# Optimization experiments

Measured on AMD Instinct MI355X. Metric: run time of the kernel, lower is better.

Reference implementation:

```python
import jax, jax.numpy as jnp
import numpy as np

PI = np.pi
ALPHA_MIN = 0.001
EXPR = 10  # mixture expressivity

B, D = 8192, 1024
T = D // 2  # transformed sites (odd indices); conditioner sites are even indices


def setup_inputs() -> dict:
    key = jax.random.key(0)
    k0, k1, k2 = jax.random.split(key, 3)
    z = jax.random.uniform(k0, (B, D), dtype=jnp.float32, minval=0.05, maxval=2 * PI - 0.05)
    H = 1024
    W1 = jax.random.normal(k1, (2 * T, H), dtype=jnp.float32) * (1.0 / np.sqrt(2 * T))
    b1 = jnp.zeros((H,), dtype=jnp.float32)
    W2 = jax.random.normal(k2, (H, T * EXPR * 3), dtype=jnp.float32) * (1.0 / np.sqrt(H))
    b2 = jnp.zeros((T * EXPR * 3,), dtype=jnp.float32)
    return {"z": z, "W1": W1, "b1": b1, "W2": W2, "b2": b2}


def _conditioner(cond, W1, b1, W2, b2):
    # angle embedding -> MLP -> (alpha, beta, rho) per transformed site / mixture comp
    feat = jnp.concatenate([jnp.cos(cond), jnp.sin(cond)], axis=-1)  # [B, 2T]
    h = jax.nn.relu(feat @ W1 + b1)
    out = (h @ W2 + b2).reshape(cond.shape[0], T, EXPR, 3)
    alpha = jax.nn.softplus(out[..., 0]) + ALPHA_MIN          # [B,T,E] >= alpha_min
    beta = out[..., 1]                                        # [B,T,E]
    rho = jax.nn.softmax(out[..., 2], axis=-1)                # [B,T,E] simplex
    return alpha, beta, rho


def _ncp(phi, alpha, beta, rho):
    # NCP diffeomorphism on (0, 2pi): mixture of 2*atan(alpha*tan((phi-pi)/2)+beta)+pi
    x = jnp.tan(0.5 * (phi - PI))[..., None]                  # [B,T,1]
    u = alpha * x + beta                                      # [B,T,E]
    h = 2.0 * jnp.arctan(u) + PI
    out = jnp.sum(rho * h, axis=-1)                           # [B,T]
    deriv = alpha * (1.0 + x * x) / (1.0 + u * u)             # dh/dphi per comp
    logabsdet = jnp.log(jnp.sum(rho * deriv, axis=-1))        # [B,T]
    return out, logabsdet


def reference(z, W1, b1, W2, b2):
    cond = z[:, 0::2]   # conditioner_mask (even sites)
    phi = z[:, 1::2]    # transformed_mask (odd sites)
    alpha, beta, rho = _conditioner(cond, W1, b1, W2, b2)
    out, ld = _ncp(phi, alpha, beta, rho)
    z_new = z.at[:, 1::2].set(out)
    log_det = jnp.sum(ld, axis=-1)  # [B]
    return z_new, log_det
```

## Files before the change

kernel.cpp:

```cpp
#include <hip/hip_runtime.h>
#include <hip/hip_bf16.h>
#include <cstdint>

#define PI_F 3.14159265358979323846f

typedef __attribute__((ext_vector_type(8))) short bf16x8;
typedef __attribute__((ext_vector_type(4))) float f32x4;

__device__ __forceinline__ void gload_lds16(const void* g, void* l) {
  __builtin_amdgcn_global_load_lds(
      (const __attribute__((address_space(1))) void*)g,
      (__attribute__((address_space(3))) void*)l, 16, 0, 0);
}

__global__ __launch_bounds__(256) void prep_feat_kernel(
    const float* __restrict__ z, __hip_bfloat16* __restrict__ feat,
    float* __restrict__ zout, float* __restrict__ logdet)
{
  int idx = blockIdx.x * 256 + threadIdx.x;
  int b = idx >> 9, j = idx & 511;
  float2 zz = ((const float2*)z)[idx];
  feat[(size_t)b * 1024 + j]       = __float2bfloat16(cosf(zz.x));
  feat[(size_t)b * 1024 + 512 + j] = __float2bfloat16(sinf(zz.x));
  zout[(size_t)b * 1024 + 2 * j]   = zz.x;
  if (idx < 8192) logdet[idx] = 0.f;
}

__global__ __launch_bounds__(256) void transpose_bf16_kernel(
    const float* __restrict__ src, __hip_bfloat16* __restrict__ dst, int R, int C)
{
  __shared__ float tile[32][33];
  int c0 = blockIdx.x * 32, r0 = blockIdx.y * 32;
  int x = threadIdx.x, y = threadIdx.y;
  #pragma unroll
  for (int i = 0; i < 32; i += 8)
    tile[y + i][x] = src[(size_t)(r0 + y + i) * C + c0 + x];
  __syncthreads();
  #pragma unroll
  for (int i = 0; i < 32; i += 8)
    dst[(size_t)(c0 + y + i) * R + r0 + x] = __float2bfloat16(tile[x][y + i]);
}

__global__ __launch_bounds__(256, 2) void gemm1_kernel(
    const __hip_bfloat16* __restrict__ A, const __hip_bfloat16* __restrict__ Bt,
    const float* __restrict__ bias, __hip_bfloat16* __restrict__ H)
{
  __shared__ __align__(16) char smem[32768];
  const int tid = threadIdx.x;
  const int lane = tid & 63;
  const int w = tid >> 6;
  const int m0 = blockIdx.x * 128;
  const int n0 = blockIdx.y * 128;
  const int lrow = lane >> 3;
  const int scol = ((lane & 7) ^ lrow) << 4;
  const int fofs0 = ((lane >> 4) << 4) ^ ((lane & 7) << 4);
  const int arow = w * 32 + (lane & 15);
  const int brow = (lane & 15);

  f32x4 acc[2][8];
  #pragma unroll
  for (int i = 0; i < 2; ++i)
    #pragma unroll
    for (int j = 0; j < 8; ++j) acc[i][j] = (f32x4){0.f, 0.f, 0.f, 0.f};

  const char* Abase = (const char*)A + (size_t)(m0 + lrow) * 2048 + scol;
  const char* Bbase = (const char*)Bt + (size_t)(n0 + lrow) * 2048 + scol;

  for (int kt = 0; kt < 16; ++kt) {
    const int k0b = kt * 128;
    __syncthreads();
    #pragma unroll
    for (int i = 0; i < 8; ++i) {
      int c = w + i * 4;
      if (c < 16) gload_lds16(Abase + (size_t)c * 16384 + k0b, smem + c * 1024);
      else        gload_lds16(Bbase + (size_t)(c - 16) * 16384 + k0b,
                              smem + 16384 + (c - 16) * 1024);
    }
    asm volatile("s_waitcnt vmcnt(0)" ::: "memory");
    __syncthreads();
    #pragma unroll
    for (int ks = 0; ks < 2; ++ks) {
      const int fo = fofs0 ^ (ks << 6);
      bf16x8 a0 = *(const bf16x8*)(smem + arow * 128 + fo);
      bf16x8 a1 = *(const bf16x8*)(smem + (arow + 16) * 128 + fo);
      #pragma unroll
      for (int fn = 0; fn < 8; ++fn) {
        bf16x8 bb = *(const bf16x8*)(smem + 16384 + (brow + fn * 16) * 128 + fo);
        acc[0][fn] = __builtin_amdgcn_mfma_f32_16x16x32_bf16(a0, bb, acc[0][fn], 0, 0, 0);
        acc[1][fn] = __builtin_amdgcn_mfma_f32_16x16x32_bf16(a1, bb, acc[1][fn], 0, 0, 0);
      }
    }
  }
  #pragma unroll
  for (int fn = 0; fn < 8; ++fn) {
    int ncol = n0 + fn * 16 + (lane & 15);
    float bv = bias[ncol];
    #pragma unroll
    for (int mf = 0; mf < 2; ++mf) {
      int mrow = m0 + w * 32 + mf * 16 + ((lane >> 4) << 2);
      #pragma unroll
      for (int j = 0; j < 4; ++j) {
        float v = fmaxf(acc[mf][fn][j] + bv, 0.f);
        H[(size_t)(mrow + j) * 1024 + ncol] = __float2bfloat16(v);
      }
    }
  }
}

__global__ __launch_bounds__(256, 2) void gemm2_ncp_kernel(
    const __hip_bfloat16* __restrict__ Hin, const __hip_bfloat16* __restrict__ W2t,
    const float* __restrict__ b2, const float* __restrict__ zin,
    float* __restrict__ zout, float* __restrict__ logdet)
{
  __shared__ __align__(16) char smem[47232];
  const int tid = threadIdx.x;
  const int lane = tid & 63;
  const int w = tid >> 6;
  const int m0 = blockIdx.x * 128;
  const int n0 = blockIdx.y * 240;
  const int lrow = lane >> 3;
  const int scol = ((lane & 7) ^ lrow) << 4;
  const int fofs0 = ((lane >> 4) << 4) ^ ((lane & 7) << 4);
  const int arow = w * 32 + (lane & 15);
  const int brow = (lane & 15);

  f32x4 acc[2][15];
  #pragma unroll
  for (int i = 0; i < 2; ++i)
    #pragma unroll
    for (int j = 0; j < 15; ++j) acc[i][j] = (f32x4){0.f, 0.f, 0.f, 0.f};

  float b2v[15];
  #pragma unroll
  for (int fn = 0; fn < 15; ++fn) b2v[fn] = b2[n0 + fn * 16 + (lane & 15)];

  const char* Abase = (const char*)Hin + (size_t)(m0 + lrow) * 2048 + scol;
  const char* Bbase = (const char*)W2t + (size_t)(n0 + lrow) * 2048 + scol;

  for (int kt = 0; kt < 16; ++kt) {
    const int k0b = kt * 128;
    __syncthreads();
    for (int c = w; c < 46; c += 4) {
      if (c < 16) gload_lds16(Abase + (size_t)c * 16384 + k0b, smem + c * 1024);
      else        gload_lds16(Bbase + (size_t)(c - 16) * 16384 + k0b,
                              smem + 16384 + (c - 16) * 1024);
    }
    asm volatile("s_waitcnt vmcnt(0)" ::: "memory");
    __syncthreads();
    #pragma unroll
    for (int ks = 0; ks < 2; ++ks) {
      const int fo = fofs0 ^ (ks << 6);
      bf16x8 a0 = *(const bf16x8*)(smem + arow * 128 + fo);
      bf16x8 a1 = *(const bf16x8*)(smem + (arow + 16) * 128 + fo);
      #pragma unroll
      for (int fn = 0; fn < 15; ++fn) {
        bf16x8 bb = *(const bf16x8*)(smem + 16384 + (brow + fn * 16) * 128 + fo);
        acc[0][fn] = __builtin_amdgcn_mfma_f32_16x16x32_bf16(a0, bb, acc[0][fn], 0, 0, 0);
        acc[1][fn] = __builtin_amdgcn_mfma_f32_16x16x32_bf16(a1, bb, acc[1][fn], 0, 0, 0);
      }
    }
  }

  const int r = tid >> 3;
  const int g = tid & 7;
  const int tglob = blockIdx.y * 8 + g;
  float* ep = (float*)(smem + 16384);

  for (int ch = 0; ch < 4; ++ch) {
    __syncthreads();
    if (w == ch) {
      #pragma unroll
      for (int mf = 0; mf < 2; ++mf) {
        const int rbase = mf * 16 + ((lane >> 4) << 2);
        #pragma unroll
        for (int fn = 0; fn < 15; ++fn) {
          const int col = fn * 16 + (lane & 15);
          #pragma unroll
          for (int j = 0; j < 4; ++j)
            ep[(rbase + j) * 241 + col] = acc[mf][fn][j] + b2v[fn];
        }
      }
    }
    __syncthreads();

    const int bidx = m0 + ch * 32 + r;
    const float* o = ep + r * 241 + g * 30;
    const float phi = zin[(size_t)bidx * 1024 + 2 * tglob + 1];
    const float x = tanf(0.5f * (phi - PI_F));
    const float x2p1 = fmaf(x, x, 1.0f);

    float q[10], mx = -1e30f;
    #pragma unroll
    for (int e = 0; e < 10; ++e) { q[e] = o[3 * e + 2]; mx = fmaxf(mx, q[e]); }

    float s = 0.f, outv = 0.f, dsum = 0.f;
    #pragma unroll
    for (int e = 0; e < 10; ++e) {
      float re = __expf(q[e] - mx);
      s += re;
      float av = o[3 * e];
      float aa = fmaxf(av, 0.f) + __logf(1.f + __expf(-fabsf(av))) + 0.001f;
      float u = fmaf(aa, x, o[3 * e + 1]);
      float hh = fmaf(2.f, atanf(u), PI_F);
      outv = fmaf(re, hh, outv);
      dsum = fmaf(re, aa * x2p1 / fmaf(u, u, 1.f), dsum);
    }
    float inv = 1.f / s;
    zout[(size_t)bidx * 1024 + 2 * tglob + 1] = outv * inv;

    float ld = __logf(dsum * inv);
    ld += __shfl_xor(ld, 1);
    ld += __shfl_xor(ld, 2);
    ld += __shfl_xor(ld, 4);
    if (g == 0) atomicAdd(&logdet[bidx], ld);
  }
}

extern "C" void kernel_launch(void* const* d_in, const int* in_sizes, int n_in,
                              void* d_out, int out_size, void* d_ws, size_t ws_size,
                              hipStream_t stream) {
  const float* z  = (const float*)d_in[0];
  const float* W1 = (const float*)d_in[1];
  const float* b1 = (const float*)d_in[2];
  const float* W2 = (const float*)d_in[3];
  const float* b2 = (const float*)d_in[4];

  float* zout   = (float*)d_out;
  float* logdet = zout + (size_t)8192 * 1024;

  char* ws = (char*)d_ws;
  __hip_bfloat16* featB = (__hip_bfloat16*)ws;
  __hip_bfloat16* hB    = (__hip_bfloat16*)(ws + 16777216);
  __hip_bfloat16* W1T   = (__hip_bfloat16*)(ws + 33554432);
  __hip_bfloat16* W2T   = (__hip_bfloat16*)(ws + 35651584);

  prep_feat_kernel<<<16384, 256, 0, stream>>>(z, featB, zout, logdet);
  transpose_bf16_kernel<<<dim3(32, 32), dim3(32, 8), 0, stream>>>(W1, W1T, 1024, 1024);
  transpose_bf16_kernel<<<dim3(480, 32), dim3(32, 8), 0, stream>>>(W2, W2T, 1024, 15360);
  gemm1_kernel<<<dim3(64, 8), 256, 0, stream>>>(featB, W1T, b1, hB);
  gemm2_ncp_kernel<<<dim3(64, 64), 256, 0, stream>>>(hB, W2T, b2, z, zout, logdet);
}
```

Before: 553.9 us.

## Pad W2 to 32 columns per site and pipeline gemm2 with 4-stage LDS buffering

Pads W2's transposed layout so each transformed site occupies 32 output columns, giving power-of-two 256x256 tiles per block. The gemm2 kernel now uses 512 threads, a 4-deep asynchronous global-to-LDS pipeline with BK=32, an 8x4 MFMA fragment layout per wave and priority hints, replacing the single-buffered load-then-compute loop. The epilogue uses a swizzled LDS staging layout and reduces the per-row log-det in LDS before one atomic per row. The cost is a small amount of wasted MFMA work on padding columns and heavy LDS use (128 KB) that limits occupancy.

```diff
diff --git a/kernel.cpp b/kernel.cpp
--- a/kernel.cpp
+++ b/kernel.cpp
@@ -39,6 +39,22 @@
   #pragma unroll
   for (int i = 0; i < 32; i += 8)
     dst[(size_t)(c0 + y + i) * R + r0 + x] = __float2bfloat16(tile[x][y + i]);
+}
+
+__global__ __launch_bounds__(256) void transpose_w2_pad_kernel(
+    const float* __restrict__ W2, __hip_bfloat16* __restrict__ dst)
+{
+  __shared__ float tile[32][33];
+  int t = blockIdx.x;
+  int k0 = blockIdx.y * 32;
+  int x = threadIdx.x, y = threadIdx.y;
+  #pragma unroll
+  for (int i = 0; i < 32; i += 8)
+    tile[y + i][x] = (x < 30) ? W2[(size_t)(k0 + y + i) * 15360 + t * 30 + x] : 0.f;
+  __syncthreads();
+  #pragma unroll
+  for (int i = 0; i < 32; i += 8)
+    dst[(size_t)(t * 32 + y + i) * 1024 + k0 + x] = __float2bfloat16(tile[x][y + i]);
 }
 
 __global__ __launch_bounds__(256, 2) void gemm1_kernel(
@@ -107,112 +123,162 @@
   }
 }
 
-__global__ __launch_bounds__(256, 2) void gemm2_ncp_kernel(
+__global__ __launch_bounds__(512, 2) void gemm2_ncp_kernel(
     const __hip_bfloat16* __restrict__ Hin, const __hip_bfloat16* __restrict__ W2t,
     const float* __restrict__ b2, const float* __restrict__ zin,
     float* __restrict__ zout, float* __restrict__ logdet)
 {
-  __shared__ __align__(16) char smem[47232];
+  __shared__ __align__(16) char smem[131072];
   const int tid = threadIdx.x;
   const int lane = tid & 63;
   const int w = tid >> 6;
-  const int m0 = blockIdx.x * 128;
-  const int n0 = blockIdx.y * 240;
-  const int lrow = lane >> 3;
-  const int scol = ((lane & 7) ^ lrow) << 4;
-  const int fofs0 = ((lane >> 4) << 4) ^ ((lane & 7) << 4);
-  const int arow = w * 32 + (lane & 15);
-  const int brow = (lane & 15);
-
-  f32x4 acc[2][15];
-  #pragma unroll
-  for (int i = 0; i < 2; ++i)
-    #pragma unroll
-    for (int j = 0; j < 15; ++j) acc[i][j] = (f32x4){0.f, 0.f, 0.f, 0.f};
-
-  float b2v[15];
-  #pragma unroll
-  for (int fn = 0; fn < 15; ++fn) b2v[fn] = b2[n0 + fn * 16 + (lane & 15)];
-
-  const char* Abase = (const char*)Hin + (size_t)(m0 + lrow) * 2048 + scol;
-  const char* Bbase = (const char*)W2t + (size_t)(n0 + lrow) * 2048 + scol;
-
-  for (int kt = 0; kt < 16; ++kt) {
-    const int k0b = kt * 128;
-    __syncthreads();
-    for (int c = w; c < 46; c += 4) {
-      if (c < 16) gload_lds16(Abase + (size_t)c * 16384 + k0b, smem + c * 1024);
-      else        gload_lds16(Bbase + (size_t)(c - 16) * 16384 + k0b,
-                              smem + 16384 + (c - 16) * 1024);
-    }
-    asm volatile("s_waitcnt vmcnt(0)" ::: "memory");
-    __syncthreads();
-    #pragma unroll
-    for (int ks = 0; ks < 2; ++ks) {
-      const int fo = fofs0 ^ (ks << 6);
-      bf16x8 a0 = *(const bf16x8*)(smem + arow * 128 + fo);
-      bf16x8 a1 = *(const bf16x8*)(smem + (arow + 16) * 128 + fo);
-      #pragma unroll
-      for (int fn = 0; fn < 15; ++fn) {
-        bf16x8 bb = *(const bf16x8*)(smem + 16384 + (brow + fn * 16) * 128 + fo);
-        acc[0][fn] = __builtin_amdgcn_mfma_f32_16x16x32_bf16(a0, bb, acc[0][fn], 0, 0, 0);
-        acc[1][fn] = __builtin_amdgcn_mfma_f32_16x16x32_bf16(a1, bb, acc[1][fn], 0, 0, 0);
-      }
-    }
-  }
-
-  const int r = tid >> 3;
-  const int g = tid & 7;
+  const int wr = w >> 2;
+  const int wc = w & 3;
+  const int m0 = blockIdx.x * 256;
+  const int n0 = blockIdx.y * 256;
+
+  const char* gA = (const char*)Hin + (size_t)(m0 + w * 16 + (lane >> 2)) * 2048 + (lane & 3) * 16;
+  const char* gB = (const char*)W2t + (size_t)(n0 + w * 16 + (lane >> 2)) * 2048 + (lane & 3) * 16;
+  const int ldsw = w * 1024;
+
+  const int abase = (wr * 128 + (lane & 15)) * 64 + (lane >> 4) * 16;
+  const int bbase = (wc * 64  + (lane & 15)) * 64 + (lane >> 4) * 16 + 16384;
+
+  auto stageA = [&](int ts) {
+    char* q = smem + ((ts & 3) << 15);
+    gload_lds16(gA + ts * 64,          q + ldsw);
+    gload_lds16(gA + 262144 + ts * 64, q + 8192 + ldsw);
+  };
+  auto stageB = [&](int ts) {
+    char* q = smem + ((ts & 3) << 15);
+    gload_lds16(gB + ts * 64,          q + 16384 + ldsw);
+    gload_lds16(gB + 262144 + ts * 64, q + 24576 + ldsw);
+  };
+
+  f32x4 acc[8][4];
+  #pragma unroll
+  for (int i = 0; i < 8; ++i)
+    #pragma unroll
+    for (int j = 0; j < 4; ++j) acc[i][j] = (f32x4){0.f, 0.f, 0.f, 0.f};
+
+  stageA(0); stageB(0); stageA(1); stageB(1); stageA(2); stageB(2);
+
+  for (int t = 0; t < 32; ++t) {
+    asm volatile("s_waitcnt vmcnt(8)" ::: "memory");
+    __builtin_amdgcn_s_barrier();
+
+    const char* LA = smem + ((t & 3) << 15);
+    int ts = t + 3; if (ts > 31) ts = 31;
+
+    bf16x8 bfr[4], afr[4];
+    #pragma unroll
+    for (int nf = 0; nf < 4; ++nf)
+      bfr[nf] = *(const bf16x8*)(LA + bbase + nf * 1024);
+    #pragma unroll
+    for (int mf = 0; mf < 4; ++mf)
+      afr[mf] = *(const bf16x8*)(LA + abase + mf * 1024);
+    if (t < 31) stageA(ts);
+    __builtin_amdgcn_s_setprio(1);
+    #pragma unroll
+    for (int mf = 0; mf < 4; ++mf)
+      #pragma unroll
+      for (int nf = 0; nf < 4; ++nf)
+        acc[mf][nf] = __builtin_amdgcn_mfma_f32_16x16x32_bf16(afr[mf], bfr[nf], acc[mf][nf], 0, 0, 0);
+    __builtin_amdgcn_s_setprio(0);
+
+    bf16x8 afr2[4];
+    #pragma unroll
+    for (int mf = 0; mf < 4; ++mf)
+      afr2[mf] = *(const bf16x8*)(LA + abase + (mf + 4) * 1024);
+    if (t < 31) stageB(ts);
+    __builtin_amdgcn_s_setprio(1);
+    #pragma unroll
+    for (int mf = 0; mf < 4; ++mf)
+      #pragma unroll
+      for (int nf = 0; nf < 4; ++nf)
+        acc[mf + 4][nf] = __builtin_amdgcn_mfma_f32_16x16x32_bf16(afr2[mf], bfr[nf], acc[mf + 4][nf], 0, 0, 0);
+    __builtin_amdgcn_s_setprio(0);
+  }
+
+  asm volatile("s_waitcnt vmcnt(0)" ::: "memory");
+  __builtin_amdgcn_s_barrier();
+
+  float* ep  = (float*)smem;
+  float* ldp = (float*)(smem + 67584);
+
+  float b2v[4];
+  #pragma unroll
+  for (int nf = 0; nf < 4; ++nf) {
+    int cglob = n0 + wc * 64 + nf * 16 + (lane & 15);
+    int tg = cglob >> 5, jj = cglob & 31;
+    b2v[nf] = (jj < 30) ? b2[tg * 30 + jj] : 0.f;
+  }
+
+  const int r = lane;
+  const int g = w;
   const int tglob = blockIdx.y * 8 + g;
-  float* ep = (float*)(smem + 16384);
-
-  for (int ch = 0; ch < 4; ++ch) {
-    __syncthreads();
-    if (w == ch) {
-      #pragma unroll
-      for (int mf = 0; mf < 2; ++mf) {
-        const int rbase = mf * 16 + ((lane >> 4) << 2);
+
+  for (int pair = 0; pair < 4; ++pair) {
+    __syncthreads();
+    if (wr == (pair >> 1)) {
+      const int mb = (pair & 1) * 4;
+      #pragma unroll
+      for (int mfl = 0; mfl < 4; ++mfl) {
         #pragma unroll
-        for (int fn = 0; fn < 15; ++fn) {
-          const int col = fn * 16 + (lane & 15);
+        for (int j = 0; j < 4; ++j) {
+          const int row = mfl * 16 + ((lane >> 4) << 2) + j;
+          const int rk = ((row >> 2) & 7) << 3;
+          float* eprow = ep + row * 264;
           #pragma unroll
-          for (int j = 0; j < 4; ++j)
-            ep[(rbase + j) * 241 + col] = acc[mf][fn][j] + b2v[fn];
+          for (int nf = 0; nf < 4; ++nf) {
+            const int col = wc * 64 + nf * 16 + (lane & 15);
+            eprow[col ^ rk] = acc[mb + mfl][nf][j] + b2v[nf];
+          }
         }
       }
     }
     __syncthreads();
 
-    const int bidx = m0 + ch * 32 + r;
-    const float* o = ep + r * 241 + g * 30;
+    float o[32];
+    const int key = ((r >> 2) & 7) << 3;
+    #pragma unroll
+    for (int k = 0; k < 8; ++k) {
+      f32x4 v = *(const f32x4*)(ep + r * 264 + ((g * 32 + 4 * k) ^ key));
+      o[4 * k + 0] = v[0]; o[4 * k + 1] = v[1];
+      o[4 * k + 2] = v[2]; o[4 * k + 3] = v[3];
+    }
+
+    const int bidx = m0 + pair * 64 + r;
     const float phi = zin[(size_t)bidx * 1024 + 2 * tglob + 1];
     const float x = tanf(0.5f * (phi - PI_F));
     const float x2p1 = fmaf(x, x, 1.0f);
 
-    float q[10], mx = -1e30f;
-    #pragma unroll
-    for (int e = 0; e < 10; ++e) { q[e] = o[3 * e + 2]; mx = fmaxf(mx, q[e]); }
+    float mx = -1e30f;
+    #pragma unroll
+    for (int e = 0; e < 10; ++e) mx = fmaxf(mx, o[3 * e + 2]);
 
     float s = 0.f, outv = 0.f, dsum = 0.f;
     #pragma unroll
     for (int e = 0; e < 10; ++e) {
-      float re = __expf(q[e] - mx);
+      float re = __expf(o[3 * e + 2] - mx);
       s += re;
       float av = o[3 * e];
       float aa = fmaxf(av, 0.f) + __logf(1.f + __expf(-fabsf(av))) + 0.001f;
       float u = fmaf(aa, x, o[3 * e + 1]);
-      float hh = fmaf(2.f, atanf(u), PI_F);
-      outv = fmaf(re, hh, outv);
+      outv = fmaf(re, fmaf(2.f, atanf(u), PI_F), outv);
       dsum = fmaf(re, aa * x2p1 / fmaf(u, u, 1.f), dsum);
     }
     float inv = 1.f / s;
     zout[(size_t)bidx * 1024 + 2 * tglob + 1] = outv * inv;
-
-    float ld = __logf(dsum * inv);
-    ld += __shfl_xor(ld, 1);
-    ld += __shfl_xor(ld, 2);
-    ld += __shfl_xor(ld, 4);
-    if (g == 0) atomicAdd(&logdet[bidx], ld);
+    ldp[g * 68 + r] = __logf(dsum * inv);
+
+    __syncthreads();
+    if (tid < 64) {
+      float sld = 0.f;
+      #pragma unroll
+      for (int gg = 0; gg < 8; ++gg) sld += ldp[gg * 68 + tid];
+      atomicAdd(&logdet[m0 + pair * 64 + tid], sld);
+    }
   }
 }
 
@@ -229,14 +295,14 @@
   float* logdet = zout + (size_t)8192 * 1024;
 
   char* ws = (char*)d_ws;
-  __hip_bfloat16* featB = (__hip_bfloat16*)ws;
-  __hip_bfloat16* hB    = (__hip_bfloat16*)(ws + 16777216);
-  __hip_bfloat16* W1T   = (__hip_bfloat16*)(ws + 33554432);
-  __hip_bfloat16* W2T   = (__hip_bfloat16*)(ws + 35651584);
+  __hip_bfloat16* hB    = (__hip_bfloat16*)ws;
+  __hip_bfloat16* W1T   = (__hip_bfloat16*)(ws + 16777216);
+  __hip_bfloat16* featB = (__hip_bfloat16*)(ws + 33554432);
+  __hip_bfloat16* W2Tp  = (__hip_bfloat16*)(ws + 33554432);
 
   prep_feat_kernel<<<16384, 256, 0, stream>>>(z, featB, zout, logdet);
   transpose_bf16_kernel<<<dim3(32, 32), dim3(32, 8), 0, stream>>>(W1, W1T, 1024, 1024);
-  transpose_bf16_kernel<<<dim3(480, 32), dim3(32, 8), 0, stream>>>(W2, W2T, 1024, 15360);
   gemm1_kernel<<<dim3(64, 8), 256, 0, stream>>>(featB, W1T, b1, hB);
-  gemm2_ncp_kernel<<<dim3(64, 64), 256, 0, stream>>>(hB, W2T, b2, z, zout, logdet);
-}
+  transpose_w2_pad_kernel<<<dim3(512, 32), dim3(32, 8), 0, stream>>>(W2, W2Tp);
+  gemm2_ncp_kernel<<<dim3(32, 64), 512, 0, stream>>>(hB, W2Tp, b2, z, zout, logdet);
+}
```

Result: slower. 772.4 us (+39.4%).
